# Performance work log

Hardware: AMD Instinct MI355X
Metric: run time of the kernel (lower is better)

The kernel has to match this reference:

```python
import jax, jax.numpy as jnp
import numpy as np

D_K = 64  # per-head dim used for the 1/sqrt(d_k) scaling


def setup_inputs() -> dict:
    key = jax.random.key(0)
    k1, k2, k3, k4 = jax.random.split(key, 4)
    B, H, Lq, NB, NT, D = 4, 8, 512, 32, 128, 64
    q = jax.random.normal(k1, (B, H, Lq, D), dtype=jnp.float32)
    k = jax.random.normal(k2, (B, NB, H, NT, D), dtype=jnp.float32)
    v = jax.random.normal(k3, (B, NB, H, NT, D), dtype=jnp.float32)
    attn_s = jax.random.uniform(k4, (B, H, Lq, NB), dtype=jnp.float32)
    return {"q": q, "k": k, "v": v, "attn_s": attn_s}


def reference(q, k, v, attn_s):
    # q: [B,H,Lq,D]; k,v: [B,NB,H,NT,D]; attn_s: [B,H,Lq,NB]
    B, NB, H, NT, D = k.shape
    Lq = q.shape[2]
    scale = 1.0 / jnp.sqrt(jnp.asarray(D_K, dtype=q.dtype))
    # block-wise QK scores: [B,NB,H,Lq,NT] (q broadcast over blocks instead of expand+matmul)
    attn = jnp.einsum('bhqd,bnhtd->bnhqt', q * scale, k)
    weights = jax.nn.softmax(attn, axis=-1)            # per-block softmax over tokens
    attn_w = jnp.transpose(weights, (0, 2, 3, 1, 4))    # [B,H,Lq,NB,NT]
    attn_w = attn_w * attn_s[..., None]                 # sentence-level reweighting
    attn_w = attn_w.reshape(B, H, Lq, NB * NT)          # concat blocks (dropout p=0 -> identity)
    v_w = jnp.transpose(v, (0, 2, 1, 3, 4)).reshape(B, H, NB * NT, D)
    out = jnp.matmul(attn_w, v_w)                       # [B,H,Lq,D]
    out = jnp.transpose(out, (0, 2, 1, 3)).reshape(B, Lq, H * D)
    return out, attn_w
```

## Files before the change

kernel.cpp:

```cpp
#include <hip/hip_runtime.h>
#include <stdint.h>

constexpr int CB=4, CH=8, CLQ=512, CNB=32, CNT=128, CD=64;
constexpr int QT=16;
constexpr int PSTR=36;
constexpr int OSTR=68;

typedef __attribute__((ext_vector_type(8))) short short8;
typedef __attribute__((ext_vector_type(4))) float f32x4;

union Frag { uint32_t u[4]; short8 s8; };

__device__ inline uint32_t fb(float x){ union{float f;uint32_t u;} v; v.f=x; return v.u; }
__device__ inline float uf(uint32_t u){ union{float f;uint32_t u;} v; v.u=u; return v.f; }
__device__ inline uint32_t packhi(float a, float b){
    return (fb(b) & 0xffff0000u) | (fb(a) >> 16);
}

__device__ inline f32x4 mfma_bf16(const Frag& a, const Frag& b, f32x4 c){
    return __builtin_amdgcn_mfma_f32_16x16x32_bf16(a.s8, b.s8, c, 0, 0, 0);
}

__global__ __launch_bounds__(256, 4)
void sdpa_mfma_kernel(const float* __restrict__ qg, const float* __restrict__ kg,
                      const float* __restrict__ vg, const float* __restrict__ sg,
                      float* __restrict__ outg, float* __restrict__ awg)
{
    __shared__ float pbuf[4 * QT * PSTR];
    __shared__ float sums[2][64];
    __shared__ float as_t[CNB * QT];
    __shared__ float obuf[4 * QT * OSTR];

    const int tid  = threadIdx.x;
    const int wave = tid >> 6;
    const int lane = tid & 63;
    const int l15  = lane & 15;
    const int q8   = lane >> 4;

    const int bid = blockIdx.x;
    const int qt  = bid & 31;
    const int bh  = bid >> 5;
    const int b   = bh >> 3;
    const int h   = bh & 7;
    const int q0  = qt * QT;

    {
        const float* sbase = sg + ((size_t)bh * CLQ + q0) * CNB;
        #pragma unroll
        for (int e = 0; e < 2; ++e) {
            int idx = tid + e * 256;
            int r = idx >> 5, n = idx & 31;
            as_t[n * QT + r] = sbase[r * CNB + n];
        }
    }

    Frag qhi[2], qlo[2];
    {
        const float* qrow = qg + ((size_t)bh * CLQ + q0 + l15) * CD;
        #pragma unroll
        for (int s = 0; s < 2; ++s) {
            f32x4 a = *(const f32x4*)&qrow[s*32 + q8*8];
            f32x4 c = *(const f32x4*)&qrow[s*32 + q8*8 + 4];
            float e[8] = {a[0]*0.125f, a[1]*0.125f, a[2]*0.125f, a[3]*0.125f,
                          c[0]*0.125f, c[1]*0.125f, c[2]*0.125f, c[3]*0.125f};
            #pragma unroll
            for (int p = 0; p < 4; ++p) {
                float e0 = e[2*p], e1 = e[2*p+1];
                qhi[s].u[p] = packhi(e0, e1);
                float h0 = uf(fb(e0) & 0xffff0000u);
                float h1 = uf(fb(e1) & 0xffff0000u);
                qlo[s].u[p] = packhi(e0 - h0, e1 - h1);
            }
        }
    }

    f32x4 O[4];
    #pragma unroll
    for (int cd = 0; cd < 4; ++cd) O[cd] = (f32x4){0.f,0.f,0.f,0.f};

    float* pw = &pbuf[wave * QT * PSTR];

    for (int n = 0; n < CNB; ++n) {
        const float* kb = kg + ((size_t)((b*CNB + n)*CH + h)) * CNT * CD;
        const float* vb = vg + ((size_t)((b*CNB + n)*CH + h)) * CNT * CD + wave*32*CD;

        f32x4 S[2];
        #pragma unroll
        for (int c = 0; c < 2; ++c) {
            const float* kr = kb + (size_t)(wave*32 + c*16 + l15) * CD;
            Frag khi[2], klo[2];
            #pragma unroll
            for (int s = 0; s < 2; ++s) {
                f32x4 a = *(const f32x4*)&kr[s*32 + q8*8];
                f32x4 d = *(const f32x4*)&kr[s*32 + q8*8 + 4];
                float e[8] = {a[0],a[1],a[2],a[3],d[0],d[1],d[2],d[3]};
                #pragma unroll
                for (int p = 0; p < 4; ++p) {
                    float e0 = e[2*p], e1 = e[2*p+1];
                    khi[s].u[p] = packhi(e0, e1);
                    float h0 = uf(fb(e0) & 0xffff0000u);
                    float h1 = uf(fb(e1) & 0xffff0000u);
                    klo[s].u[p] = packhi(e0 - h0, e1 - h1);
                }
            }
            f32x4 acc = (f32x4){0.f,0.f,0.f,0.f};
            acc = mfma_bf16(qhi[0], khi[0], acc);
            acc = mfma_bf16(qhi[1], khi[1], acc);
            acc = mfma_bf16(qlo[0], khi[0], acc);
            acc = mfma_bf16(qlo[1], khi[1], acc);
            acc = mfma_bf16(qhi[0], klo[0], acc);
            acc = mfma_bf16(qhi[1], klo[1], acc);
            S[c] = acc;
        }

        float E0[4], E1[4], ps[4];
        #pragma unroll
        for (int r = 0; r < 4; ++r) {
            E0[r] = __expf(S[0][r]);
            E1[r] = __expf(S[1][r]);
            ps[r] = E0[r] + E1[r];
        }
        #pragma unroll
        for (int off = 1; off <= 8; off <<= 1) {
            #pragma unroll
            for (int r = 0; r < 4; ++r) ps[r] += __shfl_xor(ps[r], off, 64);
        }
        if (l15 == 0) {
            f32x4 t = {ps[0], ps[1], ps[2], ps[3]};
            *(f32x4*)&sums[n & 1][wave*16 + q8*4] = t;
        }
        __syncthreads();

        f32x4 d4 = (f32x4){0.f,0.f,0.f,0.f};
        #pragma unroll
        for (int wv = 0; wv < 4; ++wv)
            d4 += *(const f32x4*)&sums[n & 1][wv*16 + q8*4];
        const f32x4 asv = *(const f32x4*)&as_t[n*QT + q8*4];

        float fac[4];
        #pragma unroll
        for (int r = 0; r < 4; ++r) fac[r] = asv[r] / d4[r];

        #pragma unroll
        for (int r = 0; r < 4; ++r) {
            pw[(q8*4 + r)*PSTR + l15]      = E0[r] * fac[r];
            pw[(q8*4 + r)*PSTR + 16 + l15] = E1[r] * fac[r];
        }

        #pragma unroll
        for (int i = 0; i < 2; ++i) {
            int idx = lane + i*64;
            int row = idx >> 3, c4 = idx & 7;
            f32x4 pv = *(const f32x4*)&pw[row*PSTR + c4*4];
            *(f32x4*)&awg[(((size_t)bh*CLQ + q0 + row)*CNB + n)*CNT + wave*32 + c4*4] = pv;
        }

        Frag phi;
        {
            f32x4 a = *(const f32x4*)&pw[l15*PSTR + q8*8];
            f32x4 c = *(const f32x4*)&pw[l15*PSTR + q8*8 + 4];
            float e[8] = {a[0],a[1],a[2],a[3],c[0],c[1],c[2],c[3]};
            #pragma unroll
            for (int p = 0; p < 4; ++p) phi.u[p] = packhi(e[2*p], e[2*p+1]);
        }

        #pragma unroll
        for (int cd = 0; cd < 4; ++cd) {
            float vf[8];
            #pragma unroll
            for (int j = 0; j < 8; ++j)
                vf[j] = vb[(q8*8 + j)*CD + cd*16 + l15];
            Frag vh;
            #pragma unroll
            for (int p = 0; p < 4; ++p) vh.u[p] = packhi(vf[2*p], vf[2*p+1]);
            O[cd] = mfma_bf16(phi, vh, O[cd]);
        }
    }

    {
        float* ow = &obuf[wave * QT * OSTR];
        #pragma unroll
        for (int cd = 0; cd < 4; ++cd)
            #pragma unroll
            for (int r = 0; r < 4; ++r)
                ow[(q8*4 + r)*OSTR + cd*16 + l15] = O[cd][r];
    }
    __syncthreads();
    {
        int r = tid >> 4, dq = tid & 15;
        f32x4 acc = (f32x4){0.f,0.f,0.f,0.f};
        #pragma unroll
        for (int wv = 0; wv < 4; ++wv)
            acc += *(const f32x4*)&obuf[wv*QT*OSTR + r*OSTR + dq*4];
        *(f32x4*)&outg[((size_t)b*CLQ + q0 + r)*(CH*CD) + h*CD + dq*4] = acc;
    }
}

extern "C" void kernel_launch(void* const* d_in, const int* in_sizes, int n_in,
                              void* d_out, int out_size, void* d_ws, size_t ws_size,
                              hipStream_t stream) {
    const float* q = (const float*)d_in[0];
    const float* k = (const float*)d_in[1];
    const float* v = (const float*)d_in[2];
    const float* s = (const float*)d_in[3];
    float* out = (float*)d_out;
    float* aw  = out + (size_t)CB * CLQ * CH * CD;

    const int grid = CB * CH * (CLQ / QT);
    sdpa_mfma_kernel<<<grid, 256, 0, stream>>>(q, k, v, s, out, aw);
}
```

Measured before the change: 489.6 us.

## Use single fp16 MFMA and assign whole key blocks per wave

Replaces the three-term bf16 hi/lo split for QK (six MFMAs per tile) with one fp16 conversion and two fp16 MFMAs, and converts P and V to fp16. Each wave now owns an entire key block, so the per-block softmax sum is done within the wave using shuffles and the per-iteration __syncthreads disappears. It also swizzles the block index, stores P in LDS as fp16, and reuses that buffer for the final output reduction. The aim is to cut MFMA count, conversion ALU work and barrier stalls. In exchange, QK scores lose precision (fp16 with round-toward-zero) and the attention-weight stores become scalar.

Result: slower. 616.1 us (+25.8%).

```diff
diff --git a/kernel.cpp b/kernel.cpp
--- a/kernel.cpp
+++ b/kernel.cpp
@@ -3,33 +3,22 @@
 
 constexpr int CB=4, CH=8, CLQ=512, CNB=32, CNT=128, CD=64;
 constexpr int QT=16;
-constexpr int PSTR=36;
+constexpr int PSTR16=136;
 constexpr int OSTR=68;
 
-typedef __attribute__((ext_vector_type(8))) short short8;
+typedef __attribute__((ext_vector_type(8))) __fp16 half8;
+typedef __attribute__((ext_vector_type(2))) __fp16 half2v;
 typedef __attribute__((ext_vector_type(4))) float f32x4;
 
-union Frag { uint32_t u[4]; short8 s8; };
-
-__device__ inline uint32_t fb(float x){ union{float f;uint32_t u;} v; v.f=x; return v.u; }
-__device__ inline float uf(uint32_t u){ union{float f;uint32_t u;} v; v.u=u; return v.f; }
-__device__ inline uint32_t packhi(float a, float b){
-    return (fb(b) & 0xffff0000u) | (fb(a) >> 16);
-}
-
-__device__ inline f32x4 mfma_bf16(const Frag& a, const Frag& b, f32x4 c){
-    return __builtin_amdgcn_mfma_f32_16x16x32_bf16(a.s8, b.s8, c, 0, 0, 0);
-}
+union HFrag { uint32_t u[4]; half8 h8; half2v h2[4]; };
 
 __global__ __launch_bounds__(256, 4)
 void sdpa_mfma_kernel(const float* __restrict__ qg, const float* __restrict__ kg,
                       const float* __restrict__ vg, const float* __restrict__ sg,
                       float* __restrict__ outg, float* __restrict__ awg)
 {
-    __shared__ float pbuf[4 * QT * PSTR];
-    __shared__ float sums[2][64];
-    __shared__ float as_t[CNB * QT];
-    __shared__ float obuf[4 * QT * OSTR];
+    __shared__ __align__(16) __fp16 pbuf[4 * QT * PSTR16];
+    __shared__ __align__(16) float as_t[CNB * QT];
 
     const int tid  = threadIdx.x;
     const int wave = tid >> 6;
@@ -37,7 +26,8 @@
     const int l15  = lane & 15;
     const int q8   = lane >> 4;
 
-    const int bid = blockIdx.x;
+    const int bid0 = blockIdx.x;
+    const int bid  = (bid0 & 7) * 128 + (bid0 >> 3);
     const int qt  = bid & 31;
     const int bh  = bid >> 5;
     const int b   = bh >> 3;
@@ -54,23 +44,17 @@
         }
     }
 
-    Frag qhi[2], qlo[2];
+    HFrag qf[2];
     {
         const float* qrow = qg + ((size_t)bh * CLQ + q0 + l15) * CD;
         #pragma unroll
         for (int s = 0; s < 2; ++s) {
             f32x4 a = *(const f32x4*)&qrow[s*32 + q8*8];
             f32x4 c = *(const f32x4*)&qrow[s*32 + q8*8 + 4];
-            float e[8] = {a[0]*0.125f, a[1]*0.125f, a[2]*0.125f, a[3]*0.125f,
-                          c[0]*0.125f, c[1]*0.125f, c[2]*0.125f, c[3]*0.125f};
-            #pragma unroll
-            for (int p = 0; p < 4; ++p) {
-                float e0 = e[2*p], e1 = e[2*p+1];
-                qhi[s].u[p] = packhi(e0, e1);
-                float h0 = uf(fb(e0) & 0xffff0000u);
-                float h1 = uf(fb(e1) & 0xffff0000u);
-                qlo[s].u[p] = packhi(e0 - h0, e1 - h1);
-            }
+            qf[s].h2[0] = __builtin_amdgcn_cvt_pkrtz(a[0]*0.125f, a[1]*0.125f);
+            qf[s].h2[1] = __builtin_amdgcn_cvt_pkrtz(a[2]*0.125f, a[3]*0.125f);
+            qf[s].h2[2] = __builtin_amdgcn_cvt_pkrtz(c[0]*0.125f, c[1]*0.125f);
+            qf[s].h2[3] = __builtin_amdgcn_cvt_pkrtz(c[2]*0.125f, c[3]*0.125f);
         }
     }
 
@@ -78,107 +62,87 @@
     #pragma unroll
     for (int cd = 0; cd < 4; ++cd) O[cd] = (f32x4){0.f,0.f,0.f,0.f};
 
-    float* pw = &pbuf[wave * QT * PSTR];
+    __fp16* pw = &pbuf[wave * QT * PSTR16];
 
-    for (int n = 0; n < CNB; ++n) {
+    __syncthreads();
+
+    #pragma unroll 1
+    for (int i = 0; i < 8; ++i) {
+        const int n = (i << 2) | wave;
         const float* kb = kg + ((size_t)((b*CNB + n)*CH + h)) * CNT * CD;
-        const float* vb = vg + ((size_t)((b*CNB + n)*CH + h)) * CNT * CD + wave*32*CD;
+        const float* vb = vg + ((size_t)((b*CNB + n)*CH + h)) * CNT * CD;
 
-        f32x4 S[2];
+        float Ev[8][4];
         #pragma unroll
-        for (int c = 0; c < 2; ++c) {
-            const float* kr = kb + (size_t)(wave*32 + c*16 + l15) * CD;
-            Frag khi[2], klo[2];
+        for (int c = 0; c < 8; ++c) {
+            const float* kr = kb + (size_t)(c*16 + l15) * CD;
+            HFrag kf[2];
             #pragma unroll
             for (int s = 0; s < 2; ++s) {
                 f32x4 a = *(const f32x4*)&kr[s*32 + q8*8];
                 f32x4 d = *(const f32x4*)&kr[s*32 + q8*8 + 4];
-                float e[8] = {a[0],a[1],a[2],a[3],d[0],d[1],d[2],d[3]};
-                #pragma unroll
-                for (int p = 0; p < 4; ++p) {
-                    float e0 = e[2*p], e1 = e[2*p+1];
-                    khi[s].u[p] = packhi(e0, e1);
-                    float h0 = uf(fb(e0) & 0xffff0000u);
-                    float h1 = uf(fb(e1) & 0xffff0000u);
-                    klo[s].u[p] = packhi(e0 - h0, e1 - h1);
-                }
+                kf[s].h2[0] = __builtin_amdgcn_cvt_pkrtz(a[0], a[1]);
+                kf[s].h2[1] = __builtin_amdgcn_cvt_pkrtz(a[2], a[3]);
+                kf[s].h2[2] = __builtin_amdgcn_cvt_pkrtz(d[0], d[1]);
+                kf[s].h2[3] = __builtin_amdgcn_cvt_pkrtz(d[2], d[3]);
             }
             f32x4 acc = (f32x4){0.f,0.f,0.f,0.f};
-            acc = mfma_bf16(qhi[0], khi[0], acc);
-            acc = mfma_bf16(qhi[1], khi[1], acc);
-            acc = mfma_bf16(qlo[0], khi[0], acc);
-            acc = mfma_bf16(qlo[1], khi[1], acc);
-            acc = mfma_bf16(qhi[0], klo[0], acc);
-            acc = mfma_bf16(qhi[1], klo[1], acc);
-            S[c] = acc;
+            acc = __builtin_amdgcn_mfma_f32_16x16x32_f16(qf[0].h8, kf[0].h8, acc, 0, 0, 0);
+            acc = __builtin_amdgcn_mfma_f32_16x16x32_f16(qf[1].h8, kf[1].h8, acc, 0, 0, 0);
+            #pragma unroll
+            for (int r = 0; r < 4; ++r) Ev[c][r] = __expf(acc[r]);
         }
 
-        float E0[4], E1[4], ps[4];
+        float ps[4];
         #pragma unroll
-        for (int r = 0; r < 4; ++r) {
-            E0[r] = __expf(S[0][r]);
-            E1[r] = __expf(S[1][r]);
-            ps[r] = E0[r] + E1[r];
-        }
+        for (int r = 0; r < 4; ++r)
+            ps[r] = ((Ev[0][r]+Ev[1][r]) + (Ev[2][r]+Ev[3][r]))
+                  + ((Ev[4][r]+Ev[5][r]) + (Ev[6][r]+Ev[7][r]));
         #pragma unroll
         for (int off = 1; off <= 8; off <<= 1) {
             #pragma unroll
             for (int r = 0; r < 4; ++r) ps[r] += __shfl_xor(ps[r], off, 64);
         }
-        if (l15 == 0) {
-            f32x4 t = {ps[0], ps[1], ps[2], ps[3]};
-            *(f32x4*)&sums[n & 1][wave*16 + q8*4] = t;
-        }
-        __syncthreads();
 
-        f32x4 d4 = (f32x4){0.f,0.f,0.f,0.f};
-        #pragma unroll
-        for (int wv = 0; wv < 4; ++wv)
-            d4 += *(const f32x4*)&sums[n & 1][wv*16 + q8*4];
         const f32x4 asv = *(const f32x4*)&as_t[n*QT + q8*4];
-
         float fac[4];
         #pragma unroll
-        for (int r = 0; r < 4; ++r) fac[r] = asv[r] / d4[r];
+        for (int r = 0; r < 4; ++r) fac[r] = asv[r] * __builtin_amdgcn_rcpf(ps[r]);
 
+        float* aw0 = awg + (((size_t)bh*CLQ + q0 + q8*4)*CNB + n)*CNT + l15;
+        __fp16* pwb = pw + (q8*4)*PSTR16 + l15;
         #pragma unroll
         for (int r = 0; r < 4; ++r) {
-            pw[(q8*4 + r)*PSTR + l15]      = E0[r] * fac[r];
-            pw[(q8*4 + r)*PSTR + 16 + l15] = E1[r] * fac[r];
+            #pragma unroll
+            for (int c = 0; c < 8; ++c) {
+                float wv = Ev[c][r] * fac[r];
+                aw0[(size_t)r*(CNB*CNT) + c*16] = wv;
+                pwb[r*PSTR16 + c*16] = (__fp16)wv;
+            }
         }
 
         #pragma unroll
-        for (int i = 0; i < 2; ++i) {
-            int idx = lane + i*64;
-            int row = idx >> 3, c4 = idx & 7;
-            f32x4 pv = *(const f32x4*)&pw[row*PSTR + c4*4];
-            *(f32x4*)&awg[(((size_t)bh*CLQ + q0 + row)*CNB + n)*CNT + wave*32 + c4*4] = pv;
-        }
-
-        Frag phi;
-        {
-            f32x4 a = *(const f32x4*)&pw[l15*PSTR + q8*8];
-            f32x4 c = *(const f32x4*)&pw[l15*PSTR + q8*8 + 4];
-            float e[8] = {a[0],a[1],a[2],a[3],c[0],c[1],c[2],c[3]};
+        for (int ks = 0; ks < 4; ++ks) {
+            HFrag pa;
+            pa.h8 = *(const half8*)&pw[l15*PSTR16 + ks*32 + q8*8];
+            const float* vrow = vb + (size_t)(ks*32 + q8*8)*CD + l15;
             #pragma unroll
-            for (int p = 0; p < 4; ++p) phi.u[p] = packhi(e[2*p], e[2*p+1]);
-        }
-
-        #pragma unroll
-        for (int cd = 0; cd < 4; ++cd) {
-            float vf[8];
-            #pragma unroll
-            for (int j = 0; j < 8; ++j)
-                vf[j] = vb[(q8*8 + j)*CD + cd*16 + l15];
-            Frag vh;
-            #pragma unroll
-            for (int p = 0; p < 4; ++p) vh.u[p] = packhi(vf[2*p], vf[2*p+1]);
-            O[cd] = mfma_bf16(phi, vh, O[cd]);
+            for (int cd = 0; cd < 4; ++cd) {
+                HFrag vf;
+                #pragma unroll
+                for (int p = 0; p < 4; ++p) {
+                    float v0 = vrow[(2*p)*CD + cd*16];
+                    float v1 = vrow[(2*p+1)*CD + cd*16];
+                    vf.h2[p] = __builtin_amdgcn_cvt_pkrtz(v0, v1);
+                }
+                O[cd] = __builtin_amdgcn_mfma_f32_16x16x32_f16(pa.h8, vf.h8, O[cd], 0, 0, 0);
+            }
         }
     }
 
+    float* obase = (float*)pbuf;
     {
-        float* ow = &obuf[wave * QT * OSTR];
+        float* ow = obase + wave * QT * OSTR;
         #pragma unroll
         for (int cd = 0; cd < 4; ++cd)
             #pragma unroll
@@ -191,7 +155,7 @@
         f32x4 acc = (f32x4){0.f,0.f,0.f,0.f};
         #pragma unroll
         for (int wv = 0; wv < 4; ++wv)
-            acc += *(const f32x4*)&obuf[wv*QT*OSTR + r*OSTR + dq*4];
+            acc += *(const f32x4*)&obase[wv*QT*OSTR + r*OSTR + dq*4];
         *(f32x4*)&outg[((size_t)b*CLQ + q0 + r)*(CH*CD) + h*CD + dq*4] = acc;
     }
 }
```
